# Performance work log

Measured on AMD Instinct MI355X. Metric: run time of the kernel, lower is better.

Reference implementation:

```python
import jax, jax.numpy as jnp
import numpy as np

B, S, X = 4, 1024, 1024
C, D = 8, 2          # num_channels, coordinate_dim
WIDTH, DEPTH = 16, 4


def setup_inputs() -> dict:
    key = jax.random.key(0)
    ks = jax.random.split(key, 8)
    scale = 1.0 / np.sqrt(WIDTH)
    return {
        "yu": jax.random.normal(ks[0], (B, S, C + D), dtype=jnp.float32),
        "x": jax.random.normal(ks[1], (B, X, D), dtype=jnp.float32),
        "W_in": jax.random.normal(ks[2], (1, WIDTH), dtype=jnp.float32),
        "b_in": jax.random.normal(ks[3], (WIDTH,), dtype=jnp.float32) * 0.1,
        "W_hid": jax.random.normal(ks[4], (DEPTH, WIDTH, WIDTH), dtype=jnp.float32) * scale,
        "b_hid": jax.random.normal(ks[5], (DEPTH, WIDTH), dtype=jnp.float32) * 0.1,
        "W_out": jax.random.normal(ks[6], (WIDTH, 1), dtype=jnp.float32) * scale,
        "b_out": jax.random.normal(ks[7], (1,), dtype=jnp.float32) * 0.1,
    }


def reference(yu, x, W_in, b_in, W_hid, b_hid, W_out, b_out):
    # split sensor positions y and sensor values u
    y = yu[:, :, -D:]           # (B, S, D)
    u = yu[:, :, :C]            # (B, S, C)
    # pairwise squared distances between eval points x and sensors y
    diff = x[:, None, :, :] - y[:, :, None, :]   # (B, S, X, D)
    r = jnp.sum(diff * diff, axis=-1)            # (B, S, X)
    # DeepResidualNetwork(1 -> 1): Linear, DEPTH x [tanh(Linear)+skip], Linear
    h = r[..., None] * W_in[0] + b_in            # (B, S, X, WIDTH)

    def res_layer(h, wb):
        w, b = wb
        return jnp.tanh(h @ w + b) + h, None

    h, _ = jax.lax.scan(res_layer, h, (W_hid, b_hid))
    k = jnp.squeeze(h @ W_out, -1) + b_out[0]    # (B, S, X)
    # Monte-Carlo integral over sensors
    return jnp.einsum('bsx,bsc->bxc', k, u) / S  # (B, X, C)
```

## Files before the change

### kernel.cpp

```cpp
#include <hip/hip_runtime.h>
#include <math.h>

#define BB 4
#define SS 1024
#define XX 1024
#define CC 8
#define DD 2
#define WIDTH 16
#define DEPTH 4

#define NLUT 4096
#define RSCALE 16.0f
#define GQ 8

__device__ __forceinline__ float fast_tanh(float v) {
    float ax = __builtin_fabsf(v);
    float e  = __builtin_amdgcn_exp2f(ax * -2.885390081777927f);
    float t  = fmaf(2.0f, __builtin_amdgcn_rcpf(1.0f + e), -1.0f);
    return __builtin_copysignf(t, v);
}

__global__ __launch_bounds__(64) void build_lut(
    const float* __restrict__ W_in, const float* __restrict__ b_in,
    const float* __restrict__ W_hid, const float* __restrict__ b_hid,
    const float* __restrict__ W_out, const float* __restrict__ b_out,
    float* __restrict__ lut)
{
    const int idx = blockIdx.x * 64 + threadIdx.x;
    const float r = (float)idx * (1.0f / RSCALE);

    float h[WIDTH];
#pragma unroll
    for (int j = 0; j < WIDTH; ++j) h[j] = fmaf(r, W_in[j], b_in[j]);

#pragma unroll
    for (int l = 0; l < DEPTH; ++l) {
        const float* W  = W_hid + l * WIDTH * WIDTH;
        const float* bb = b_hid + l * WIDTH;
        float pre[WIDTH];
#pragma unroll
        for (int j = 0; j < WIDTH; ++j) pre[j] = bb[j];
#pragma unroll
        for (int i = 0; i < WIDTH; ++i) {
            const float hi = h[i];
#pragma unroll
            for (int j = 0; j < WIDTH; ++j)
                pre[j] = fmaf(hi, W[i * WIDTH + j], pre[j]);
        }
#pragma unroll
        for (int j = 0; j < WIDTH; ++j) h[j] += fast_tanh(pre[j]);
    }

    float k = b_out[0];
#pragma unroll
    for (int j = 0; j < WIDTH; ++j) k = fmaf(h[j], W_out[j], k);
    lut[idx] = k;
}

__global__ __launch_bounds__(256) void ccl_main(
    const float* __restrict__ yu,
    const float* __restrict__ x,
    const float* __restrict__ lut_g,
    float* __restrict__ out)
{
    __shared__ float lut_s[NLUT];
    __shared__ float red[GQ * 4 * CC];

    const int bx   = blockIdx.x;
    const int b    = bx / (XX / GQ);
    const int xi0  = (bx % (XX / GQ)) * GQ;
    const int tid  = threadIdx.x;
    const int lane = tid & 63;
    const int wv   = tid >> 6;

    {
        const float4* src = reinterpret_cast<const float4*>(lut_g);
        float4*       dst = reinterpret_cast<float4*>(lut_s);
#pragma unroll
        for (int i = 0; i < NLUT / 4 / 256; ++i)
            dst[tid + i * 256] = src[tid + i * 256];
    }

    const float* yub = yu + (size_t)b * SS * (CC + DD);
    float2 yp[4];
    float  up[4][CC];
#pragma unroll
    for (int i = 0; i < 4; ++i) {
        const int s = tid + i * 256;
        const float2* row = reinterpret_cast<const float2*>(yub + (size_t)s * (CC + DD));
        float2 a0 = row[0], a1 = row[1], a2 = row[2], a3 = row[3];
        yp[i] = row[4];
        up[i][0] = a0.x; up[i][1] = a0.y; up[i][2] = a1.x; up[i][3] = a1.y;
        up[i][4] = a2.x; up[i][5] = a2.y; up[i][6] = a3.x; up[i][7] = a3.y;
    }

    float qx[GQ], qy[GQ];
    {
        const float* xp = x + ((size_t)b * XX + xi0) * DD;
#pragma unroll
        for (int q = 0; q < GQ; ++q) { qx[q] = xp[2 * q]; qy[q] = xp[2 * q + 1]; }
    }

    __syncthreads();

    const bool b0 = (lane & 1) != 0;
    const bool b1 = (lane & 2) != 0;
    const bool b2 = (lane & 4) != 0;

    float vq[GQ];

#pragma unroll
    for (int q = 0; q < GQ; ++q) {
        float acc[CC];
#pragma unroll
        for (int c = 0; c < CC; ++c) acc[c] = 0.0f;

#pragma unroll
        for (int i = 0; i < 4; ++i) {
            const float d0 = qx[q] - yp[i].x;
            const float d1 = qy[q] - yp[i].y;
            const float r  = fmaf(d0, d0, d1 * d1);

            float rf = r * RSCALE;
            int   ix = (int)rf;
            ix = min(ix, NLUT - 2);
            const float w  = rf - (float)ix;
            const float f0 = lut_s[ix];
            const float f1 = lut_s[ix + 1];
            const float k  = fmaf(w, f1 - f0, f0);

#pragma unroll
            for (int c = 0; c < CC; ++c) acc[c] = fmaf(k, up[i][c], acc[c]);
        }

        float m[4];
#pragma unroll
        for (int i = 0; i < 4; ++i) {
            float u = b0 ? acc[2 * i + 1] : acc[2 * i];
            float w = b0 ? acc[2 * i]     : acc[2 * i + 1];
            m[i] = u + __shfl_xor(w, 1, 64);
        }
        float n[2];
#pragma unroll
        for (int j = 0; j < 2; ++j) {
            float u = b1 ? m[2 * j + 1] : m[2 * j];
            float w = b1 ? m[2 * j]     : m[2 * j + 1];
            n[j] = u + __shfl_xor(w, 2, 64);
        }
        {
            float u = b2 ? n[1] : n[0];
            float w = b2 ? n[0] : n[1];
            float p = u + __shfl_xor(w, 4, 64);
            p += __shfl_xor(p, 8, 64);
            p += __shfl_xor(p, 16, 64);
            p += __shfl_xor(p, 32, 64);
            vq[q] = p;
        }
    }

    if (lane < CC) {
#pragma unroll
        for (int q = 0; q < GQ; ++q)
            red[(q * 4 + wv) * CC + lane] = vq[q];
    }
    __syncthreads();
    if (tid < GQ * CC) {
        const int q = tid >> 3;
        const int c = tid & 7;
        const float v = red[(q * 4 + 0) * CC + c] + red[(q * 4 + 1) * CC + c] +
                        red[(q * 4 + 2) * CC + c] + red[(q * 4 + 3) * CC + c];
        out[((size_t)b * XX + xi0 + q) * CC + c] = v * (1.0f / SS);
    }
}

extern "C" void kernel_launch(void* const* d_in, const int* in_sizes, int n_in,
                              void* d_out, int out_size, void* d_ws, size_t ws_size,
                              hipStream_t stream) {
    const float* yu    = (const float*)d_in[0];
    const float* x     = (const float*)d_in[1];
    const float* W_in  = (const float*)d_in[2];
    const float* b_in  = (const float*)d_in[3];
    const float* W_hid = (const float*)d_in[4];
    const float* b_hid = (const float*)d_in[5];
    const float* W_out = (const float*)d_in[6];
    const float* b_out = (const float*)d_in[7];
    float* out = (float*)d_out;
    float* lut = (float*)d_ws;

    build_lut<<<dim3(NLUT / 64), dim3(64), 0, stream>>>(
        W_in, b_in, W_hid, b_hid, W_out, b_out, lut);

    ccl_main<<<dim3(BB * XX / GQ), dim3(256), 0, stream>>>(yu, x, lut, out);
}
```

Baseline: 85.47 us.

## Pack LUT value/slope pairs, prescale coordinates, use DPP and transposed reduction

The shared LUT now holds (value, next-minus-value) float2 pairs, so each interpolation does one 64-bit LDS read and one FMA instead of two reads and a subtract. Coordinates are prescaled by sqrt(RSCALE) at load time, which removes the per-pair multiply on r. Cross-lane reductions use DPP moves for the xor-1, xor-2 and xor-8 steps. The final cross-q reduction is transposed so that each lane ends up holding one (q, c) result, which replaces the per-q xor-8/16/32 shuffles and simplifies the LDS write. The costs are double the LUT LDS footprint and a slightly different rounding of r from the prescaling.

After: 86.41 us. About the same (+1.1%).

```diff
diff --git a/kernel.cpp b/kernel.cpp
--- a/kernel.cpp
+++ b/kernel.cpp
@@ -11,6 +11,7 @@
 
 #define NLUT 4096
 #define RSCALE 16.0f
+#define RSQRT_SCALE 4.0f
 #define GQ 8
 
 __device__ __forceinline__ float fast_tanh(float v) {
@@ -18,6 +19,12 @@
     float e  = __builtin_amdgcn_exp2f(ax * -2.885390081777927f);
     float t  = fmaf(2.0f, __builtin_amdgcn_rcpf(1.0f + e), -1.0f);
     return __builtin_copysignf(t, v);
+}
+
+template <int CTRL>
+__device__ __forceinline__ float dpp_mov(float w) {
+    return __int_as_float(
+        __builtin_amdgcn_mov_dpp(__float_as_int(w), CTRL, 0xF, 0xF, true));
 }
 
 __global__ __launch_bounds__(64) void build_lut(
@@ -63,8 +70,8 @@
     const float* __restrict__ lut_g,
     float* __restrict__ out)
 {
-    __shared__ float lut_s[NLUT];
-    __shared__ float red[GQ * 4 * CC];
+    __shared__ __align__(16) float2 lut2_s[NLUT];
+    __shared__ float red[4 * 64];
 
     const int bx   = blockIdx.x;
     const int b    = bx / (XX / GQ);
@@ -75,10 +82,15 @@
 
     {
         const float4* src = reinterpret_cast<const float4*>(lut_g);
-        float4*       dst = reinterpret_cast<float4*>(lut_s);
-#pragma unroll
-        for (int i = 0; i < NLUT / 4 / 256; ++i)
-            dst[tid + i * 256] = src[tid + i * 256];
+        float4*       d4  = reinterpret_cast<float4*>(lut2_s);
+#pragma unroll
+        for (int i = 0; i < NLUT / 4 / 256; ++i) {
+            const int g = tid + i * 256;
+            float4 v = src[g];
+            float nxt = (g < NLUT / 4 - 1) ? lut_g[4 * g + 4] : v.w;
+            d4[2 * g]     = make_float4(v.x, v.y - v.x, v.y, v.z - v.y);
+            d4[2 * g + 1] = make_float4(v.z, v.w - v.z, v.w, nxt - v.w);
+        }
     }
 
     const float* yub = yu + (size_t)b * SS * (CC + DD);
@@ -89,7 +101,8 @@
         const int s = tid + i * 256;
         const float2* row = reinterpret_cast<const float2*>(yub + (size_t)s * (CC + DD));
         float2 a0 = row[0], a1 = row[1], a2 = row[2], a3 = row[3];
-        yp[i] = row[4];
+        float2 yv = row[4];
+        yp[i] = make_float2(yv.x * RSQRT_SCALE, yv.y * RSQRT_SCALE);
         up[i][0] = a0.x; up[i][1] = a0.y; up[i][2] = a1.x; up[i][3] = a1.y;
         up[i][4] = a2.x; up[i][5] = a2.y; up[i][6] = a3.x; up[i][7] = a3.y;
     }
@@ -98,14 +111,20 @@
     {
         const float* xp = x + ((size_t)b * XX + xi0) * DD;
 #pragma unroll
-        for (int q = 0; q < GQ; ++q) { qx[q] = xp[2 * q]; qy[q] = xp[2 * q + 1]; }
+        for (int q = 0; q < GQ; ++q) {
+            qx[q] = xp[2 * q]     * RSQRT_SCALE;
+            qy[q] = xp[2 * q + 1] * RSQRT_SCALE;
+        }
     }
 
     __syncthreads();
 
-    const bool b0 = (lane & 1) != 0;
-    const bool b1 = (lane & 2) != 0;
-    const bool b2 = (lane & 4) != 0;
+    const bool b0 = (lane & 1)  != 0;
+    const bool b1 = (lane & 2)  != 0;
+    const bool b2 = (lane & 4)  != 0;
+    const bool b3 = (lane & 8)  != 0;
+    const bool b4 = (lane & 16) != 0;
+    const bool b5 = (lane & 32) != 0;
 
     float vq[GQ];
 
@@ -119,15 +138,13 @@
         for (int i = 0; i < 4; ++i) {
             const float d0 = qx[q] - yp[i].x;
             const float d1 = qy[q] - yp[i].y;
-            const float r  = fmaf(d0, d0, d1 * d1);
-
-            float rf = r * RSCALE;
-            int   ix = (int)rf;
+            const float rf = fmaf(d0, d0, d1 * d1);
+
+            int ix = (int)rf;
             ix = min(ix, NLUT - 2);
             const float w  = rf - (float)ix;
-            const float f0 = lut_s[ix];
-            const float f1 = lut_s[ix + 1];
-            const float k  = fmaf(w, f1 - f0, f0);
+            const float2 fd = lut2_s[ix];
+            const float k  = fmaf(w, fd.y, fd.x);
 
 #pragma unroll
             for (int c = 0; c < CC; ++c) acc[c] = fmaf(k, up[i][c], acc[c]);
@@ -138,37 +155,49 @@
         for (int i = 0; i < 4; ++i) {
             float u = b0 ? acc[2 * i + 1] : acc[2 * i];
             float w = b0 ? acc[2 * i]     : acc[2 * i + 1];
-            m[i] = u + __shfl_xor(w, 1, 64);
+            m[i] = u + dpp_mov<0xB1>(w);
         }
         float n[2];
 #pragma unroll
         for (int j = 0; j < 2; ++j) {
             float u = b1 ? m[2 * j + 1] : m[2 * j];
             float w = b1 ? m[2 * j]     : m[2 * j + 1];
-            n[j] = u + __shfl_xor(w, 2, 64);
+            n[j] = u + dpp_mov<0x4E>(w);
         }
         {
             float u = b2 ? n[1] : n[0];
             float w = b2 ? n[0] : n[1];
-            float p = u + __shfl_xor(w, 4, 64);
-            p += __shfl_xor(p, 8, 64);
-            p += __shfl_xor(p, 16, 64);
-            p += __shfl_xor(p, 32, 64);
-            vq[q] = p;
-        }
-    }
-
-    if (lane < CC) {
-#pragma unroll
-        for (int q = 0; q < GQ; ++q)
-            red[(q * 4 + wv) * CC + lane] = vq[q];
-    }
+            vq[q] = u + __shfl_xor(w, 4, 64);
+        }
+    }
+
+    float m2[4];
+#pragma unroll
+    for (int i = 0; i < 4; ++i) {
+        float u = b3 ? vq[2 * i + 1] : vq[2 * i];
+        float w = b3 ? vq[2 * i]     : vq[2 * i + 1];
+        m2[i] = u + dpp_mov<0x128>(w);
+    }
+    float n2[2];
+#pragma unroll
+    for (int j = 0; j < 2; ++j) {
+        float u = b4 ? m2[2 * j + 1] : m2[2 * j];
+        float w = b4 ? m2[2 * j]     : m2[2 * j + 1];
+        n2[j] = u + __shfl_xor(w, 16, 64);
+    }
+    float p2;
+    {
+        float u = b5 ? n2[1] : n2[0];
+        float w = b5 ? n2[0] : n2[1];
+        p2 = u + __shfl_xor(w, 32, 64);
+    }
+
+    red[wv * 64 + lane] = p2;
     __syncthreads();
-    if (tid < GQ * CC) {
+    if (tid < 64) {
         const int q = tid >> 3;
         const int c = tid & 7;
-        const float v = red[(q * 4 + 0) * CC + c] + red[(q * 4 + 1) * CC + c] +
-                        red[(q * 4 + 2) * CC + c] + red[(q * 4 + 3) * CC + c];
+        const float v = red[tid] + red[64 + tid] + red[128 + tid] + red[192 + tid];
         out[((size_t)b * XX + xi0 + q) * CC + c] = v * (1.0f / SS);
     }
 }
```
